# Performance work log

Hardware: AMD Instinct MI355X
Metric: run time of the kernel (lower is better)

The kernel has to match this reference:

```python
import jax, jax.numpy as jnp
import numpy as np

B, S, D = 2, 4096, 2048
HEADS, HEAD_DIM = 16, 128
EPS = 1e-5


def setup_inputs() -> dict:
    key = jax.random.key(0)
    ks = jax.random.split(key, 8)
    hidden_states = jax.random.normal(ks[0], (B, S, D), dtype=jnp.float32)
    # rotary angles, broadcastable to [B, S, heads, head_dim]
    freqs_cis = jax.random.uniform(ks[1], (1, S, 1, HEAD_DIM), dtype=jnp.float32) * 6.283185
    scale = 1.0 / np.sqrt(D)
    # weights stored [in, out] (transpose of torch Linear weight)
    wq = jax.random.normal(ks[2], (D, HEADS * HEAD_DIM), dtype=jnp.float32) * scale
    wk = jax.random.normal(ks[3], (D, HEADS * HEAD_DIM), dtype=jnp.float32) * scale
    wv = jax.random.normal(ks[4], (D, HEADS * HEAD_DIM), dtype=jnp.float32) * scale
    norm_q_w = jnp.ones((HEAD_DIM,), dtype=jnp.float32)
    norm_k_w = jnp.ones((HEAD_DIM,), dtype=jnp.float32)
    w_out = jax.random.normal(ks[5], (HEADS * HEAD_DIM, D), dtype=jnp.float32) * scale
    b_out = jnp.zeros((D,), dtype=jnp.float32)
    return {"hidden_states": hidden_states, "freqs_cis": freqs_cis,
            "wq": wq, "wk": wk, "wv": wv,
            "norm_q_w": norm_q_w, "norm_k_w": norm_k_w,
            "w_out": w_out, "b_out": b_out}


def _rms_norm(x, w):
    var = jnp.mean(jnp.square(x), axis=-1, keepdims=True)
    return x * jax.lax.rsqrt(var + EPS) * w


def _apply_rotary(x, freqs_cis):
    rot_dim = freqs_cis.shape[-1]
    xr, x_pass = x[..., :rot_dim], x[..., rot_dim:]
    cos_ = jnp.cos(freqs_cis).astype(x.dtype)
    sin_ = jnp.sin(freqs_cis).astype(x.dtype)
    x1, x2 = jnp.split(xr, 2, axis=-1)
    x_rot = jnp.concatenate((-x2, x1), axis=-1)
    return jnp.concatenate((xr * cos_ + x_rot * sin_, x_pass), axis=-1)


def reference(hidden_states, freqs_cis, wq, wk, wv, norm_q_w, norm_k_w, w_out, b_out):
    b, s, _ = hidden_states.shape
    # QKV projections -> [B, S, H, Dh]
    q = (hidden_states @ wq).reshape(b, s, HEADS, HEAD_DIM)
    k = (hidden_states @ wk).reshape(b, s, HEADS, HEAD_DIM)
    v = (hidden_states @ wv).reshape(b, s, HEADS, HEAD_DIM)
    q = _rms_norm(q, norm_q_w)
    k = _rms_norm(k, norm_k_w)
    q = _apply_rotary(q, freqs_cis)
    k = _apply_rotary(k, freqs_cis)
    # SDPA with BSND layout, scale = 1/sqrt(head_dim)
    attn = jax.nn.dot_product_attention(q, k, v)  # [B, S, H, Dh]
    out = attn.reshape(b, s, HEADS * HEAD_DIM) @ w_out + b_out
    return out
```

## Files before the change

### kernel.cpp

```cpp
#include <hip/hip_runtime.h>
#include <stdint.h>


#define S_LEN  4096
#define NHEAD  16
#define HDIM   128
#define DMODEL 2048
#define MROWS  8192

typedef unsigned short u16;
typedef unsigned int   u32;
typedef __attribute__((ext_vector_type(4)))  float  f32x4;
typedef __attribute__((ext_vector_type(16))) float  f32x16;
typedef __attribute__((ext_vector_type(4)))  u16    u16x4;
typedef __attribute__((ext_vector_type(8)))  u16    u16x8;
typedef __attribute__((ext_vector_type(4)))  u32    u32x4;
typedef __attribute__((ext_vector_type(8)))  __bf16 bf16x8;

__device__ __forceinline__ u16 f2bf(float x){
  unsigned u = __builtin_bit_cast(unsigned, x);
  u += 0x7FFFu + ((u >> 16) & 1u);
  return (u16)(u >> 16);
}
__device__ __forceinline__ float bf2f(u16 b){
  unsigned u = ((unsigned)b) << 16;
  return __builtin_bit_cast(float, u);
}
__device__ __forceinline__ u32 cvtpk(float lo, float hi_){
  u32 r;
  asm("v_cvt_pk_bf16_f32 %0, %1, %2" : "=v"(r) : "v"(lo), "v"(hi_));
  return r;
}
__device__ __forceinline__ void gload16(const void* g, void* l){
  __builtin_amdgcn_global_load_lds((__attribute__((address_space(1))) void*)g,
                                   (__attribute__((address_space(3))) void*)l,
                                   16, 0, 0);
}

__global__ void k_cast_hs(const float* __restrict__ in, u16* __restrict__ out){
  size_t i = (size_t)blockIdx.x * 256 + threadIdx.x;
  const f32x4* p = (const f32x4*)in;
  f32x4 a = p[i*2], b = p[i*2+1];
  u16x8 o;
  o[0]=f2bf(a[0]); o[1]=f2bf(a[1]); o[2]=f2bf(a[2]); o[3]=f2bf(a[3]);
  o[4]=f2bf(b[0]); o[5]=f2bf(b[1]); o[6]=f2bf(b[2]); o[7]=f2bf(b[3]);
  ((u16x8*)out)[i] = o;
}

__global__ void k_transpose_w(const float* __restrict__ in, u16* __restrict__ out){
  __shared__ float t[64][65];
  const int tid = threadIdx.x;
  const int k0 = blockIdx.x * 64, n0 = blockIdx.y * 64;
#pragma unroll
  for (int it = 0; it < 4; ++it){
    int slot = it*256 + tid;
    int r = slot >> 4, c = (slot & 15) * 4;
    f32x4 v = *(const f32x4*)&in[(size_t)(k0+r)*DMODEL + n0 + c];
    t[r][c] = v[0]; t[r][c+1] = v[1]; t[r][c+2] = v[2]; t[r][c+3] = v[3];
  }
  __syncthreads();
#pragma unroll
  for (int it = 0; it < 2; ++it){
    int slot = it*256 + tid;
    int r = slot >> 3, c = (slot & 7) * 8;
    u16x8 o;
#pragma unroll
    for (int j = 0; j < 8; ++j) o[j] = f2bf(t[c+j][r]);
    *(u16x8*)&out[(size_t)(n0+r)*DMODEL + k0 + c] = o;
  }
}

__global__ void k_tables(const float* __restrict__ fr, float* __restrict__ cn,
                         float* __restrict__ sn){
  int i = blockIdx.x*256 + threadIdx.x;
  float f = fr[i];
  cn[i] = cosf(f); sn[i] = sinf(f);
}

__device__ __forceinline__ void stage_ab(const u16* __restrict__ A,
                                         const u16* __restrict__ Bt,
                                         int m0, int n0, int kt,
                                         u16* Asm, u16* Bsm, int lane, int wid){
#pragma unroll
  for (int it = 0; it < 4; ++it){
    int slot = it*256 + wid*64 + lane;
    int row = slot >> 3, cs = slot & 7;
    int ci = cs ^ (row & 7);
    gload16(A  + (size_t)(m0+row)*DMODEL + kt*64 + ci*8, Asm + (size_t)(it*256 + wid*64)*8);
    gload16(Bt + (size_t)(n0+row)*DMODEL + kt*64 + ci*8, Bsm + (size_t)(it*256 + wid*64)*8);
  }
}

__device__ __forceinline__ void gemm_loop(const u16* __restrict__ A,
                                          const u16* __restrict__ Bt,
                                          int m0, int n0,
                                          u16 (*Asm)[128*64], u16 (*Bsm)[128*64],
                                          f32x4 (&acc)[4][4], int lane, int wid){
  const int wr = wid >> 1, wc = wid & 1;
  stage_ab(A, Bt, m0, n0, 0, Asm[0], Bsm[0], lane, wid);
#pragma unroll 1
  for (int kt = 0; kt < DMODEL/64; ++kt){
    if (kt + 1 < DMODEL/64){
      stage_ab(A, Bt, m0, n0, kt + 1, Asm[(kt + 1) & 1], Bsm[(kt + 1) & 1], lane, wid);
      asm volatile("s_waitcnt vmcnt(8)" ::: "memory");
    } else {
      asm volatile("s_waitcnt vmcnt(0)" ::: "memory");
    }
    __builtin_amdgcn_s_barrier();
    asm volatile("" ::: "memory");
    const u16* As = Asm[kt & 1];
    const u16* Bs = Bsm[kt & 1];
#pragma unroll
    for (int ks = 0; ks < 2; ++ks){
      bf16x8 af[4], bfv[4];
#pragma unroll
      for (int mt = 0; mt < 4; ++mt){
        int row = wr*64 + mt*16 + (lane & 15);
        int cs = (ks*4 + (lane >> 4)) ^ (row & 7);
        af[mt] = *(const bf16x8*)(As + ((size_t)row*8 + cs)*8);
      }
#pragma unroll
      for (int nt = 0; nt < 4; ++nt){
        int row = wc*64 + nt*16 + (lane & 15);
        int cs = (ks*4 + (lane >> 4)) ^ (row & 7);
        bfv[nt] = *(const bf16x8*)(Bs + ((size_t)row*8 + cs)*8);
      }
#pragma unroll
      for (int mt = 0; mt < 4; ++mt)
#pragma unroll
        for (int nt = 0; nt < 4; ++nt)
          acc[mt][nt] = __builtin_amdgcn_mfma_f32_16x16x32_bf16(af[mt], bfv[nt], acc[mt][nt], 0, 0, 0);
    }
    __builtin_amdgcn_s_barrier();
    asm volatile("" ::: "memory");
  }
}

__global__ __launch_bounds__(256, 2)
void k_gemm_qkv(const u16* __restrict__ A, const u16* __restrict__ Bt,
                u16* __restrict__ qkp, u16* __restrict__ vt){
  __shared__ u16 Asm[2][128*64];
  __shared__ u16 Bsm[2][128*64];
  const int lane = threadIdx.x & 63, wid = threadIdx.x >> 6;
  const int m0 = blockIdx.x * 128, n0 = blockIdx.y * 128;
  f32x4 acc[4][4] = {};
  gemm_loop(A, Bt, m0, n0, Asm, Bsm, acc, lane, wid);
  const int wr = wid >> 1, wc = wid & 1;
  if (n0 < 2*DMODEL){
#pragma unroll
    for (int mt = 0; mt < 4; ++mt)
#pragma unroll
      for (int nt = 0; nt < 4; ++nt){
        int col = n0 + wc*64 + nt*16 + (lane & 15);
#pragma unroll
        for (int r = 0; r < 4; ++r){
          int row = m0 + wr*64 + mt*16 + (lane >> 4)*4 + r;
          qkp[(size_t)row*4096 + col] = f2bf(acc[mt][nt][r]);
        }
      }
  } else {
    const int hh = (n0 - 2*DMODEL) >> 7;
    const int b  = m0 >> 12;
#pragma unroll
    for (int mt = 0; mt < 4; ++mt)
#pragma unroll
      for (int nt = 0; nt < 4; ++nt){
        u16x4 pk;
#pragma unroll
        for (int r = 0; r < 4; ++r) pk[r] = f2bf(acc[mt][nt][r]);
        int d  = wc*64 + nt*16 + (lane & 15);
        int s_ = (m0 & (S_LEN-1)) + wr*64 + mt*16 + (lane >> 4)*4;
        *(u16x4*)&vt[(((size_t)b*NHEAD + hh)*HDIM + d)*S_LEN + s_] = pk;
      }
  }
}

__global__ __launch_bounds__(256)
void k_qk_post(const u16* __restrict__ qkp, const float* __restrict__ cn,
               const float* __restrict__ sn, const float* __restrict__ wqn,
               const float* __restrict__ wkn, u16* __restrict__ Qo, u16* __restrict__ Ko){
  const int lane = threadIdx.x & 63, wid = threadIdx.x >> 6;
  const int gw = blockIdx.x*4 + wid;
  const int row = gw >> 4;
  const int h  = gw & 15;
  const int s_ = row & (S_LEN-1);
  const int b  = row >> 12;
  const float c1 = cn[s_*HDIM + lane],      c2 = cn[s_*HDIM + 64 + lane];
  const float t1 = sn[s_*HDIM + lane],      t2 = sn[s_*HDIM + 64 + lane];
  const size_t ob = (((size_t)b*NHEAD + h)*S_LEN + s_)*HDIM;
  {
    const u16* p = qkp + (size_t)row*4096 + h*HDIM;
    float x1 = bf2f(p[lane]), x2 = bf2f(p[lane+64]);
    float ss = x1*x1 + x2*x2;
#pragma unroll
    for (int m = 1; m < 64; m <<= 1) ss += __shfl_xor(ss, m);
    float rn = rsqrtf(ss*(1.0f/128.0f) + 1e-5f);
    x1 *= rn * wqn[lane]; x2 *= rn * wqn[lane+64];
    const float qs = 0.12751743f;
    Qo[ob + lane]      = f2bf((x1*c1 - x2*t1) * qs);
    Qo[ob + 64 + lane] = f2bf((x2*c2 + x1*t2) * qs);
  }
  {
    const u16* p = qkp + (size_t)row*4096 + 2048 + h*HDIM;
    float x1 = bf2f(p[lane]), x2 = bf2f(p[lane+64]);
    float ss = x1*x1 + x2*x2;
#pragma unroll
    for (int m = 1; m < 64; m <<= 1) ss += __shfl_xor(ss, m);
    float rn = rsqrtf(ss*(1.0f/128.0f) + 1e-5f);
    x1 *= rn * wkn[lane]; x2 *= rn * wkn[lane+64];
    Ko[ob + lane]      = f2bf(x1*c1 - x2*t1);
    Ko[ob + 64 + lane] = f2bf(x2*c2 + x1*t2);
  }
}

__device__ __forceinline__ void stage_kv(const u16* __restrict__ Kg,
                                         const u16* __restrict__ Vt,
                                         size_t base, int kb,
                                         u16* Ksm, u16* Vsm, int lane, int wid){
#pragma unroll
  for (int it = 0; it < 4; ++it){
    int slot = it*256 + wid*64 + lane;
    { int row = slot >> 4, cs = slot & 15, ci = cs ^ (row & 7);
      gload16(Kg + base + (size_t)(kb*64 + row)*HDIM + ci*8, Ksm + (size_t)(it*256 + wid*64)*8); }
    { int row = slot >> 3, cs = slot & 7,  ci = cs ^ (row & 7);
      gload16(Vt + base + (size_t)row*S_LEN + kb*64 + ci*8,  Vsm + (size_t)(it*256 + wid*64)*8); }
  }
}

__global__ __launch_bounds__(256, 2)
void k_attn(const u16* __restrict__ Q, const u16* __restrict__ Kg,
            const u16* __restrict__ Vt, u16* __restrict__ Og){
  __shared__ u16 Ksm[2][64*128];
  __shared__ u16 Vsm[2][128*64];
  const int lane = threadIdx.x & 63, wid = threadIdx.x >> 6;
  const int col = lane & 31, hi = lane >> 5;
  const int bh = blockIdx.y;
  const int b = bh >> 4, h = bh & 15;
  const size_t base = (size_t)bh * S_LEN * HDIM;
  const int q0 = blockIdx.x * 128;
  const int qw = q0 + wid*32;

  stage_kv(Kg, Vt, base, 0, Ksm[0], Vsm[0], lane, wid);

  bf16x8 qb[8];
  {
    const u16* qp = Q + base + (size_t)(qw + col)*HDIM + hi*8;
#pragma unroll
    for (int ks = 0; ks < 8; ++ks) qb[ks] = *(const bf16x8*)(qp + ks*16);
  }
  f32x16 acc[4] = {};
  float lsum = 0.f;
  int cur = 0;

#pragma unroll 1
  for (int kb = 0; kb < S_LEN/64; ++kb){
    if (kb + 1 < S_LEN/64){
      stage_kv(Kg, Vt, base, kb + 1, Ksm[cur ^ 1], Vsm[cur ^ 1], lane, wid);
      asm volatile("s_waitcnt vmcnt(8)" ::: "memory");
    } else {
      asm volatile("s_waitcnt vmcnt(0)" ::: "memory");
    }
    __builtin_amdgcn_s_barrier();
    asm volatile("" ::: "memory");
    const u16* Ks = Ksm[cur];
    const u16* Vs = Vsm[cur];

    f32x16 s0 = {}, s1 = {};
    __builtin_amdgcn_s_setprio(1);
#pragma unroll
    for (int ks = 0; ks < 8; ++ks){
      int slot = (ks*2 + hi);
      int r0 = col;
      bf16x8 kf0 = *(const bf16x8*)(Ks + (size_t)r0*128 + (size_t)(slot ^ (r0 & 7))*8);
      s0 = __builtin_amdgcn_mfma_f32_32x32x16_bf16(kf0, qb[ks], s0, 0, 0, 0);
      int r1 = col + 32;
      bf16x8 kf1 = *(const bf16x8*)(Ks + (size_t)r1*128 + (size_t)(slot ^ (r1 & 7))*8);
      s1 = __builtin_amdgcn_mfma_f32_32x32x16_bf16(kf1, qb[ks], s1, 0, 0, 0);
    }
    __builtin_amdgcn_s_setprio(0);

    float p0[16], p1[16];
#pragma unroll
    for (int r = 0; r < 16; ++r){
      p0[r] = __builtin_amdgcn_exp2f(s0[r]);
      p1[r] = __builtin_amdgcn_exp2f(s1[r]);
      lsum += p0[r] + p1[r];
    }
    u32 cw0[8], cw1[8];
#pragma unroll
    for (int j = 0; j < 8; ++j){
      cw0[j] = cvtpk(p0[2*j], p0[2*j+1]);
      cw1[j] = cvtpk(p1[2*j], p1[2*j+1]);
    }
    bf16x8 pa[4];
#pragma unroll
    for (int ks = 0; ks < 4; ++ks){
      const u32* cw = (ks < 2) ? cw0 : cw1;
      const int c4 = (ks & 1) * 4;
      u32 n0 = hi ? cw[c4+2] : cw[c4+0];
      u32 n1 = hi ? cw[c4+3] : cw[c4+1];
      u32 s0w = hi ? cw[c4+0] : cw[c4+2];
      u32 s1w = hi ? cw[c4+1] : cw[c4+3];
      u32 f0 = __shfl_xor((int)s0w, 32);
      u32 f1 = __shfl_xor((int)s1w, 32);
      u32x4 w;
      w[0] = hi ? f0 : n0;
      w[1] = hi ? f1 : n1;
      w[2] = hi ? n0 : f0;
      w[3] = hi ? n1 : f1;
      pa[ks] = __builtin_bit_cast(bf16x8, w);
    }

    __builtin_amdgcn_s_setprio(1);
#pragma unroll
    for (int dt = 0; dt < 4; ++dt){
      int row = dt*32 + col;
      const u16* vb = Vs + (size_t)row*64;
      int sw = row & 7;
#pragma unroll
      for (int ks = 0; ks < 4; ++ks){
        bf16x8 vf = *(const bf16x8*)(vb + (size_t)((ks*2 + hi) ^ sw)*8);
        acc[dt] = __builtin_amdgcn_mfma_f32_32x32x16_bf16(pa[ks], vf, acc[dt], 0, 0, 0);
      }
    }
    __builtin_amdgcn_s_setprio(0);
    __builtin_amdgcn_s_barrier();
    asm volatile("" ::: "memory");
    cur ^= 1;
  }

  float tot = lsum + __shfl_xor(lsum, 32);
  float inv[16];
#pragma unroll
  for (int r = 0; r < 16; ++r){
    int qr = (r & 3) + 4*hi + 8*(r >> 2);
    inv[r] = 1.0f / __shfl(tot, qr);
  }
  const size_t orow0 = (size_t)b*S_LEN + q0 + wid*32;
#pragma unroll
  for (int dt = 0; dt < 4; ++dt){
    int d = h*HDIM + dt*32 + col;
#pragma unroll
    for (int r = 0; r < 16; ++r){
      int qr = (r & 3) + 4*hi + 8*(r >> 2);
      Og[(orow0 + qr)*DMODEL + d] = f2bf(acc[dt][r] * inv[r]);
    }
  }
}

__global__ __launch_bounds__(256, 2)
void k_gemm_out(const u16* __restrict__ A, const u16* __restrict__ Bt,
                const float* __restrict__ bias, float* __restrict__ out){
  __shared__ u16 Asm[2][128*64];
  __shared__ u16 Bsm[2][128*64];
  const int lane = threadIdx.x & 63, wid = threadIdx.x >> 6;
  const int m0 = blockIdx.x * 128, n0 = blockIdx.y * 128;
  f32x4 acc[4][4] = {};
  gemm_loop(A, Bt, m0, n0, Asm, Bsm, acc, lane, wid);
  const int wr = wid >> 1, wc = wid & 1;
  float bv[4];
#pragma unroll
  for (int nt = 0; nt < 4; ++nt) bv[nt] = bias[n0 + wc*64 + nt*16 + (lane & 15)];
#pragma unroll
  for (int mt = 0; mt < 4; ++mt)
#pragma unroll
    for (int nt = 0; nt < 4; ++nt){
      int col = n0 + wc*64 + nt*16 + (lane & 15);
#pragma unroll
      for (int r = 0; r < 4; ++r){
        int row = m0 + wr*64 + mt*16 + (lane >> 4)*4 + r;
        out[(size_t)row*DMODEL + col] = acc[mt][nt][r] + bv[nt];
      }
    }
}

extern "C" void kernel_launch(void* const* d_in, const int* in_sizes, int n_in,
                              void* d_out, int out_size, void* d_ws, size_t ws_size,
                              hipStream_t stream){
  const float* hs    = (const float*)d_in[0];
  const float* freqs = (const float*)d_in[1];
  const float* wq    = (const float*)d_in[2];
  const float* wk    = (const float*)d_in[3];
  const float* wv    = (const float*)d_in[4];
  const float* nqw   = (const float*)d_in[5];
  const float* nkw   = (const float*)d_in[6];
  const float* wo    = (const float*)d_in[7];
  const float* bo    = (const float*)d_in[8];
  float* out = (float*)d_out;

  char* ws = (char*)d_ws;
  u16*   hs_bf = (u16*)(ws + 0);
  u16*   wqkvT = (u16*)(ws + 33554432);
  u16*   woutT = (u16*)(ws + 58720256);
  float* cosn  = (float*)(ws + 67108864);
  float* sinn  = (float*)(ws + 69206016);
  u16*   qkp   = (u16*)(ws + 71303168);
  u16*   vt    = (u16*)(ws + 138412032);
  u16*   kbuf  = (u16*)(ws + 171966464);
  if (ws_size < 205520896ULL) return;
  u16* qbuf = hs_bf;
  u16* attn = qkp;

  k_cast_hs    <<<8192, 256, 0, stream>>>(hs, hs_bf);
  k_transpose_w<<<dim3(32,32), 256, 0, stream>>>(wq, wqkvT);
  k_transpose_w<<<dim3(32,32), 256, 0, stream>>>(wk, wqkvT + (size_t)DMODEL*DMODEL);
  k_transpose_w<<<dim3(32,32), 256, 0, stream>>>(wv, wqkvT + (size_t)2*DMODEL*DMODEL);
  k_transpose_w<<<dim3(32,32), 256, 0, stream>>>(wo, woutT);
  k_tables     <<<2048, 256, 0, stream>>>(freqs, cosn, sinn);
  k_gemm_qkv   <<<dim3(64,48), 256, 0, stream>>>(hs_bf, wqkvT, qkp, vt);
  k_qk_post    <<<32768, 256, 0, stream>>>(qkp, cosn, sinn, nqw, nkw, qbuf, kbuf);
  k_attn       <<<dim3(32,32), 256, 0, stream>>>(qbuf, kbuf, vt, attn);
  k_gemm_out   <<<dim3(64,16), 256, 0, stream>>>(attn, woutT, bo, out);
}
```

Before: 655.6 us.

## Fuse QK RMSNorm and rotary into QKV GEMM epilogue, add XCD-aware block remap

```diff
diff --git a/kernel.cpp b/kernel.cpp
--- a/kernel.cpp
+++ b/kernel.cpp
@@ -35,6 +35,9 @@
   __builtin_amdgcn_global_load_lds((__attribute__((address_space(1))) void*)g,
                                    (__attribute__((address_space(3))) void*)l,
                                    16, 0, 0);
+}
+__device__ __forceinline__ int xcd_chunk(int bid, int nwg){
+  return (bid & 7) * (nwg >> 3) + (bid >> 3);
 }
 
 __global__ void k_cast_hs(const float* __restrict__ in, u16* __restrict__ out){
@@ -138,26 +141,79 @@
 
 __global__ __launch_bounds__(256, 2)
 void k_gemm_qkv(const u16* __restrict__ A, const u16* __restrict__ Bt,
-                u16* __restrict__ qkp, u16* __restrict__ vt){
+                const float* __restrict__ cosn, const float* __restrict__ sinn,
+                const float* __restrict__ nqw,  const float* __restrict__ nkw,
+                u16* __restrict__ Qo, u16* __restrict__ Ko, u16* __restrict__ vt){
   __shared__ u16 Asm[2][128*64];
   __shared__ u16 Bsm[2][128*64];
   const int lane = threadIdx.x & 63, wid = threadIdx.x >> 6;
-  const int m0 = blockIdx.x * 128, n0 = blockIdx.y * 128;
+  const int t  = xcd_chunk(blockIdx.x, 64*48);
+  const int m0 = (t & 63) * 128;
+  const int n0 = (t >> 6) * 128;
   f32x4 acc[4][4] = {};
   gemm_loop(A, Bt, m0, n0, Asm, Bsm, acc, lane, wid);
   const int wr = wid >> 1, wc = wid & 1;
+
   if (n0 < 2*DMODEL){
+    const bool isq = (n0 < DMODEL);
+    const int  h   = (n0 >> 7) & 15;
+    const float* w = isq ? nqw : nkw;
+    u16* dst = isq ? Qo : Ko;
+    const float qs = isq ? 0.12751743f : 1.0f;
+    float* baseF = (wid < 2) ? (float*)Asm : (float*)Bsm;
+    float* myT = baseF + (size_t)(wid  & 1) * 4096;
+    float* paT = baseF + (size_t)((wid ^ 1) & 1) * 4096;
 #pragma unroll
     for (int mt = 0; mt < 4; ++mt)
 #pragma unroll
-      for (int nt = 0; nt < 4; ++nt){
-        int col = n0 + wc*64 + nt*16 + (lane & 15);
-#pragma unroll
-        for (int r = 0; r < 4; ++r){
-          int row = m0 + wr*64 + mt*16 + (lane >> 4)*4 + r;
-          qkp[(size_t)row*4096 + col] = f2bf(acc[mt][nt][r]);
+      for (int nt = 0; nt < 4; ++nt)
+#pragma unroll
+        for (int r = 0; r < 4; ++r)
+          myT[(size_t)(mt*16 + (lane>>4)*4 + r)*64 + nt*16 + (lane & 15)] = acc[mt][nt][r];
+    __syncthreads();
+    float wo_[4], wp_[4];
+#pragma unroll
+    for (int nt = 0; nt < 4; ++nt){
+      int j = nt*16 + (lane & 15);
+      wo_[nt] = w[wc*64 + j];
+      wp_[nt] = w[(1 - wc)*64 + j];
+    }
+#pragma unroll
+    for (int mt = 0; mt < 4; ++mt){
+      float pv[4][4];
+      float rn[4];
+#pragma unroll
+      for (int r = 0; r < 4; ++r){
+        int rl = mt*16 + (lane>>4)*4 + r;
+        float s = 0.f;
+#pragma unroll
+        for (int nt = 0; nt < 4; ++nt){
+          pv[nt][r] = paT[(size_t)rl*64 + nt*16 + (lane & 15)];
+          s += acc[mt][nt][r]*acc[mt][nt][r] + pv[nt][r]*pv[nt][r];
         }
-      }
+        s += __shfl_xor(s, 1); s += __shfl_xor(s, 2);
+        s += __shfl_xor(s, 4); s += __shfl_xor(s, 8);
+        rn[r] = rsqrtf(s*(1.0f/128.0f) + 1e-5f) * qs;
+      }
+#pragma unroll
+      for (int r = 0; r < 4; ++r){
+        int row = m0 + wr*64 + mt*16 + (lane>>4)*4 + r;
+        int s_  = row & (S_LEN-1);
+        int b   = row >> 12;
+        size_t ob = (((size_t)b*NHEAD + h)*S_LEN + s_)*HDIM;
+#pragma unroll
+        for (int nt = 0; nt < 4; ++nt){
+          int j = nt*16 + (lane & 15);
+          int dout = wc*64 + j;
+          float c = cosn[s_*HDIM + dout];
+          float tt = sinn[s_*HDIM + dout];
+          float ao = acc[mt][nt][r] * rn[r] * wo_[nt];
+          float ap = pv[nt][r]      * rn[r] * wp_[nt];
+          float o  = wc ? (ao*c + ap*tt) : (ao*c - ap*tt);
+          dst[ob + dout] = f2bf(o);
+        }
+      }
+    }
   } else {
     const int hh = (n0 - 2*DMODEL) >> 7;
     const int b  = m0 >> 12;
@@ -172,44 +228,6 @@
         int s_ = (m0 & (S_LEN-1)) + wr*64 + mt*16 + (lane >> 4)*4;
         *(u16x4*)&vt[(((size_t)b*NHEAD + hh)*HDIM + d)*S_LEN + s_] = pk;
       }
-  }
-}
-
-__global__ __launch_bounds__(256)
-void k_qk_post(const u16* __restrict__ qkp, const float* __restrict__ cn,
-               const float* __restrict__ sn, const float* __restrict__ wqn,
-               const float* __restrict__ wkn, u16* __restrict__ Qo, u16* __restrict__ Ko){
-  const int lane = threadIdx.x & 63, wid = threadIdx.x >> 6;
-  const int gw = blockIdx.x*4 + wid;
-  const int row = gw >> 4;
-  const int h  = gw & 15;
-  const int s_ = row & (S_LEN-1);
-  const int b  = row >> 12;
-  const float c1 = cn[s_*HDIM + lane],      c2 = cn[s_*HDIM + 64 + lane];
-  const float t1 = sn[s_*HDIM + lane],      t2 = sn[s_*HDIM + 64 + lane];
-  const size_t ob = (((size_t)b*NHEAD + h)*S_LEN + s_)*HDIM;
-  {
-    const u16* p = qkp + (size_t)row*4096 + h*HDIM;
-    float x1 = bf2f(p[lane]), x2 = bf2f(p[lane+64]);
-    float ss = x1*x1 + x2*x2;
-#pragma unroll
-    for (int m = 1; m < 64; m <<= 1) ss += __shfl_xor(ss, m);
-    float rn = rsqrtf(ss*(1.0f/128.0f) + 1e-5f);
-    x1 *= rn * wqn[lane]; x2 *= rn * wqn[lane+64];
-    const float qs = 0.12751743f;
-    Qo[ob + lane]      = f2bf((x1*c1 - x2*t1) * qs);
-    Qo[ob + 64 + lane] = f2bf((x2*c2 + x1*t2) * qs);
-  }
-  {
-    const u16* p = qkp + (size_t)row*4096 + 2048 + h*HDIM;
-    float x1 = bf2f(p[lane]), x2 = bf2f(p[lane+64]);
-    float ss = x1*x1 + x2*x2;
-#pragma unroll
-    for (int m = 1; m < 64; m <<= 1) ss += __shfl_xor(ss, m);
-    float rn = rsqrtf(ss*(1.0f/128.0f) + 1e-5f);
-    x1 *= rn * wkn[lane]; x2 *= rn * wkn[lane+64];
-    Ko[ob + lane]      = f2bf(x1*c1 - x2*t1);
-    Ko[ob + 64 + lane] = f2bf(x2*c2 + x1*t2);
   }
 }
 
@@ -234,10 +252,11 @@
   __shared__ u16 Vsm[2][128*64];
   const int lane = threadIdx.x & 63, wid = threadIdx.x >> 6;
   const int col = lane & 31, hi = lane >> 5;
-  const int bh = blockIdx.y;
+  const int t  = xcd_chunk(blockIdx.x, 32*32);
+  const int bh = t >> 5;
+  const int q0 = (t & 31) * 128;
   const int b = bh >> 4, h = bh & 15;
   const size_t base = (size_t)bh * S_LEN * HDIM;
-  const int q0 = blockIdx.x * 128;
   const int qw = q0 + wid*32;
 
   stage_kv(Kg, Vt, base, 0, Ksm[0], Vsm[0], lane, wid);
@@ -354,7 +373,9 @@
   __shared__ u16 Asm[2][128*64];
   __shared__ u16 Bsm[2][128*64];
   const int lane = threadIdx.x & 63, wid = threadIdx.x >> 6;
-  const int m0 = blockIdx.x * 128, n0 = blockIdx.y * 128;
+  const int t  = xcd_chunk(blockIdx.x, 64*16);
+  const int m0 = (t & 63) * 128;
+  const int n0 = (t >> 6) * 128;
   f32x4 acc[4][4] = {};
   gemm_loop(A, Bt, m0, n0, Asm, Bsm, acc, lane, wid);
   const int wr = wid >> 1, wc = wid & 1;
@@ -394,12 +415,11 @@
   u16*   woutT = (u16*)(ws + 58720256);
   float* cosn  = (float*)(ws + 67108864);
   float* sinn  = (float*)(ws + 69206016);
-  u16*   qkp   = (u16*)(ws + 71303168);
+  u16*   qbuf  = (u16*)(ws + 71303168);
+  u16*   kbuf  = (u16*)(ws + 104857600);
   u16*   vt    = (u16*)(ws + 138412032);
-  u16*   kbuf  = (u16*)(ws + 171966464);
+  u16*   attn  = (u16*)(ws + 171966464);
   if (ws_size < 205520896ULL) return;
-  u16* qbuf = hs_bf;
-  u16* attn = qkp;
 
   k_cast_hs    <<<8192, 256, 0, stream>>>(hs, hs_bf);
   k_transpose_w<<<dim3(32,32), 256, 0, stream>>>(wq, wqkvT);
@@ -407,8 +427,7 @@
   k_transpose_w<<<dim3(32,32), 256, 0, stream>>>(wv, wqkvT + (size_t)2*DMODEL*DMODEL);
   k_transpose_w<<<dim3(32,32), 256, 0, stream>>>(wo, woutT);
   k_tables     <<<2048, 256, 0, stream>>>(freqs, cosn, sinn);
-  k_gemm_qkv   <<<dim3(64,48), 256, 0, stream>>>(hs_bf, wqkvT, qkp, vt);
-  k_qk_post    <<<32768, 256, 0, stream>>>(qkp, cosn, sinn, nqw, nkw, qbuf, kbuf);
-  k_attn       <<<dim3(32,32), 256, 0, stream>>>(qbuf, kbuf, vt, attn);
-  k_gemm_out   <<<dim3(64,16), 256, 0, stream>>>(attn, woutT, bo, out);
-}
+  k_gemm_qkv   <<<3072, 256, 0, stream>>>(hs_bf, wqkvT, cosn, sinn, nqw, nkw, qbuf, kbuf, vt);
+  k_attn       <<<1024, 256, 0, stream>>>(qbuf, kbuf, vt, attn);
+  k_gemm_out   <<<1024, 256, 0, stream>>>(attn, woutT, bo, out);
+}
```

Result: slower. 696.8 us (+6.3%).

## Use 32x32x16 MFMA in GEMMs and XCD-aware block mapping for attention

Applied to the files above, without the earlier changes.

```diff
diff --git a/kernel.cpp b/kernel.cpp
--- a/kernel.cpp
+++ b/kernel.cpp
@@ -36,6 +36,9 @@
                                    (__attribute__((address_space(3))) void*)l,
                                    16, 0, 0);
 }
+__device__ __forceinline__ int xcd_chunk(int bid, int nwg){
+  return (bid & 7) * (nwg >> 3) + (bid >> 3);
+}
 
 __global__ void k_cast_hs(const float* __restrict__ in, u16* __restrict__ out){
   size_t i = (size_t)blockIdx.x * 256 + threadIdx.x;
@@ -95,8 +98,9 @@
                                           const u16* __restrict__ Bt,
                                           int m0, int n0,
                                           u16 (*Asm)[128*64], u16 (*Bsm)[128*64],
-                                          f32x4 (&acc)[4][4], int lane, int wid){
+                                          f32x16 (&acc)[2][2], int lane, int wid){
   const int wr = wid >> 1, wc = wid & 1;
+  const int col = lane & 31, hi = lane >> 5;
   stage_ab(A, Bt, m0, n0, 0, Asm[0], Bsm[0], lane, wid);
 #pragma unroll 1
   for (int kt = 0; kt < DMODEL/64; ++kt){
@@ -111,25 +115,24 @@
     const u16* As = Asm[kt & 1];
     const u16* Bs = Bsm[kt & 1];
 #pragma unroll
-    for (int ks = 0; ks < 2; ++ks){
-      bf16x8 af[4], bfv[4];
-#pragma unroll
-      for (int mt = 0; mt < 4; ++mt){
-        int row = wr*64 + mt*16 + (lane & 15);
-        int cs = (ks*4 + (lane >> 4)) ^ (row & 7);
-        af[mt] = *(const bf16x8*)(As + ((size_t)row*8 + cs)*8);
-      }
-#pragma unroll
-      for (int nt = 0; nt < 4; ++nt){
-        int row = wc*64 + nt*16 + (lane & 15);
-        int cs = (ks*4 + (lane >> 4)) ^ (row & 7);
-        bfv[nt] = *(const bf16x8*)(Bs + ((size_t)row*8 + cs)*8);
-      }
-#pragma unroll
-      for (int mt = 0; mt < 4; ++mt)
-#pragma unroll
-        for (int nt = 0; nt < 4; ++nt)
-          acc[mt][nt] = __builtin_amdgcn_mfma_f32_16x16x32_bf16(af[mt], bfv[nt], acc[mt][nt], 0, 0, 0);
+    for (int ks = 0; ks < 4; ++ks){
+      const int c = ks*2 + hi;
+      bf16x8 af[2], bfv[2];
+#pragma unroll
+      for (int mt = 0; mt < 2; ++mt){
+        int row = wr*64 + mt*32 + col;
+        af[mt] = *(const bf16x8*)(As + ((size_t)row*8 + (size_t)(c ^ (row & 7)))*8);
+      }
+#pragma unroll
+      for (int nt = 0; nt < 2; ++nt){
+        int row = wc*64 + nt*32 + col;
+        bfv[nt] = *(const bf16x8*)(Bs + ((size_t)row*8 + (size_t)(c ^ (row & 7)))*8);
+      }
+#pragma unroll
+      for (int mt = 0; mt < 2; ++mt)
+#pragma unroll
+        for (int nt = 0; nt < 2; ++nt)
+          acc[mt][nt] = __builtin_amdgcn_mfma_f32_32x32x16_bf16(af[mt], bfv[nt], acc[mt][nt], 0, 0, 0);
     }
     __builtin_amdgcn_s_barrier();
     asm volatile("" ::: "memory");
@@ -142,35 +145,40 @@
   __shared__ u16 Asm[2][128*64];
   __shared__ u16 Bsm[2][128*64];
   const int lane = threadIdx.x & 63, wid = threadIdx.x >> 6;
+  const int col = lane & 31, hi = lane >> 5;
   const int m0 = blockIdx.x * 128, n0 = blockIdx.y * 128;
-  f32x4 acc[4][4] = {};
+  f32x16 acc[2][2] = {};
   gemm_loop(A, Bt, m0, n0, Asm, Bsm, acc, lane, wid);
   const int wr = wid >> 1, wc = wid & 1;
   if (n0 < 2*DMODEL){
 #pragma unroll
-    for (int mt = 0; mt < 4; ++mt)
-#pragma unroll
-      for (int nt = 0; nt < 4; ++nt){
-        int col = n0 + wc*64 + nt*16 + (lane & 15);
-#pragma unroll
-        for (int r = 0; r < 4; ++r){
-          int row = m0 + wr*64 + mt*16 + (lane >> 4)*4 + r;
-          qkp[(size_t)row*4096 + col] = f2bf(acc[mt][nt][r]);
+    for (int mt = 0; mt < 2; ++mt)
+#pragma unroll
+      for (int nt = 0; nt < 2; ++nt){
+        int cn = n0 + wc*64 + nt*32 + col;
+#pragma unroll
+        for (int r = 0; r < 16; ++r){
+          int rowm = (r & 3) + 8*(r >> 2) + 4*hi;
+          int row = m0 + wr*64 + mt*32 + rowm;
+          qkp[(size_t)row*4096 + cn] = f2bf(acc[mt][nt][r]);
         }
       }
   } else {
     const int hh = (n0 - 2*DMODEL) >> 7;
     const int b  = m0 >> 12;
 #pragma unroll
-    for (int mt = 0; mt < 4; ++mt)
-#pragma unroll
-      for (int nt = 0; nt < 4; ++nt){
-        u16x4 pk;
-#pragma unroll
-        for (int r = 0; r < 4; ++r) pk[r] = f2bf(acc[mt][nt][r]);
-        int d  = wc*64 + nt*16 + (lane & 15);
-        int s_ = (m0 & (S_LEN-1)) + wr*64 + mt*16 + (lane >> 4)*4;
-        *(u16x4*)&vt[(((size_t)b*NHEAD + hh)*HDIM + d)*S_LEN + s_] = pk;
+    for (int mt = 0; mt < 2; ++mt)
+#pragma unroll
+      for (int nt = 0; nt < 2; ++nt){
+        int d = wc*64 + nt*32 + col;
+#pragma unroll
+        for (int j = 0; j < 4; ++j){
+          u16x4 pk;
+#pragma unroll
+          for (int e = 0; e < 4; ++e) pk[e] = f2bf(acc[mt][nt][4*j + e]);
+          int s_ = (m0 & (S_LEN-1)) + wr*64 + mt*32 + 8*j + 4*hi;
+          *(u16x4*)&vt[(((size_t)b*NHEAD + hh)*HDIM + d)*S_LEN + s_] = pk;
+        }
       }
   }
 }
@@ -234,10 +242,11 @@
   __shared__ u16 Vsm[2][128*64];
   const int lane = threadIdx.x & 63, wid = threadIdx.x >> 6;
   const int col = lane & 31, hi = lane >> 5;
-  const int bh = blockIdx.y;
+  const int t  = xcd_chunk(blockIdx.x, 1024);
+  const int bh = t >> 5;
+  const int q0 = (t & 31) * 128;
   const int b = bh >> 4, h = bh & 15;
   const size_t base = (size_t)bh * S_LEN * HDIM;
-  const int q0 = blockIdx.x * 128;
   const int qw = q0 + wid*32;
 
   stage_kv(Kg, Vt, base, 0, Ksm[0], Vsm[0], lane, wid);
@@ -354,22 +363,24 @@
   __shared__ u16 Asm[2][128*64];
   __shared__ u16 Bsm[2][128*64];
   const int lane = threadIdx.x & 63, wid = threadIdx.x >> 6;
+  const int col = lane & 31, hi = lane >> 5;
   const int m0 = blockIdx.x * 128, n0 = blockIdx.y * 128;
-  f32x4 acc[4][4] = {};
+  f32x16 acc[2][2] = {};
   gemm_loop(A, Bt, m0, n0, Asm, Bsm, acc, lane, wid);
   const int wr = wid >> 1, wc = wid & 1;
-  float bv[4];
-#pragma unroll
-  for (int nt = 0; nt < 4; ++nt) bv[nt] = bias[n0 + wc*64 + nt*16 + (lane & 15)];
-#pragma unroll
-  for (int mt = 0; mt < 4; ++mt)
-#pragma unroll
-    for (int nt = 0; nt < 4; ++nt){
-      int col = n0 + wc*64 + nt*16 + (lane & 15);
-#pragma unroll
-      for (int r = 0; r < 4; ++r){
-        int row = m0 + wr*64 + mt*16 + (lane >> 4)*4 + r;
-        out[(size_t)row*DMODEL + col] = acc[mt][nt][r] + bv[nt];
+  float bv[2];
+#pragma unroll
+  for (int nt = 0; nt < 2; ++nt) bv[nt] = bias[n0 + wc*64 + nt*32 + col];
+#pragma unroll
+  for (int mt = 0; mt < 2; ++mt)
+#pragma unroll
+    for (int nt = 0; nt < 2; ++nt){
+      int cn = n0 + wc*64 + nt*32 + col;
+#pragma unroll
+      for (int r = 0; r < 16; ++r){
+        int rowm = (r & 3) + 8*(r >> 2) + 4*hi;
+        int row = m0 + wr*64 + mt*32 + rowm;
+        out[(size_t)row*DMODEL + cn] = acc[mt][nt][r] + bv[nt];
       }
     }
 }
@@ -409,6 +420,6 @@
   k_tables     <<<2048, 256, 0, stream>>>(freqs, cosn, sinn);
   k_gemm_qkv   <<<dim3(64,48), 256, 0, stream>>>(hs_bf, wqkvT, qkp, vt);
   k_qk_post    <<<32768, 256, 0, stream>>>(qkp, cosn, sinn, nqw, nkw, qbuf, kbuf);
-  k_attn       <<<dim3(32,32), 256, 0, stream>>>(qbuf, kbuf, vt, attn);
+  k_attn       <<<1024, 256, 0, stream>>>(qbuf, kbuf, vt, attn);
   k_gemm_out   <<<dim3(64,16), 256, 0, stream>>>(attn, woutT, bo, out);
 }
```

New measurement: 664.9 us. About the same (+1.4%).
